# Kernel optimization log

Hardware: AMD Instinct MI355X
Metric: run time of the kernel (lower is better)

Reference implementation:

```python
import jax, jax.numpy as jnp
import numpy as np

C, H, W = 16, 512, 512
HID = 128
N_STEPS = 8


def setup_inputs() -> dict:
    key = jax.random.key(0)
    k1, k2, k3 = jax.random.split(key, 3)
    state = jax.random.normal(k1, (C, H, W), dtype=jnp.float32)
    # MLP params: 5*C = 80 gathered features -> HID -> C delta channels
    W1 = jax.random.normal(k2, (5 * C, HID), dtype=jnp.float32) * (1.0 / np.sqrt(5 * C))
    b1 = jnp.zeros((HID,), dtype=jnp.float32)
    W2 = jax.random.normal(k3, (HID, C), dtype=jnp.float32) * (1.0 / np.sqrt(HID))
    b2 = jnp.zeros((C,), dtype=jnp.float32)
    return {"state": state, "W1": W1, "b1": b1, "W2": W2, "b2": b2, "n_steps": N_STEPS}


def _neighbor_idx(n):
    i = jnp.arange(n)
    minus = jnp.maximum(i - 1, 0)          # clamp at low edge (cy==0 -> 0)
    plus = jnp.where(i == n - 1, 0, i + 1)  # WRAP to 0 at high edge (original quirk)
    return minus, plus


def reference(state, W1, b1, W2, b2, n_steps):
    c, h, w = state.shape
    up, down = _neighbor_idx(h)
    left, right = _neighbor_idx(w)

    def step(s, _):
        # von-Neumann gather: (5C, H, W), feature order [center, up, down, left, right]
        feats = jnp.concatenate(
            [s, s[:, up, :], s[:, down, :], s[:, :, left], s[:, :, right]], axis=0)
        x = feats.reshape(5 * c, h * w).T        # (HW, 5C)
        hdn = jax.nn.relu(x @ W1 + b1)           # (HW, HID)
        delta = (hdn @ W2 + b2).T.reshape(c, h, w)
        s_new = s + delta
        s_new = s_new.at[0].set(s[0])            # channel 0 snapshot restore
        return s_new, None

    out, _ = jax.lax.scan(step, state, None, length=n_steps)
    return out
```

## Files before the change

### kernel.cpp

```cpp
#include <hip/hip_runtime.h>
#include <hip/hip_bf16.h>

#define HH 512
#define WW 512
#define CC 16
#define HIDN 128
#define HWSZ (HH*WW)

typedef __attribute__((ext_vector_type(8))) short short8;
typedef __attribute__((ext_vector_type(4))) short short4v;
typedef __attribute__((ext_vector_type(4))) float float4v;

__device__ __forceinline__ short to_bf16(float f){
    __hip_bfloat16 h = __float2bfloat16(f);
    return __builtin_bit_cast(short, h);
}

__global__ void __launch_bounds__(256) prep_kernel(
    const float* __restrict__ W1, const float* __restrict__ W2,
    short* __restrict__ w1t, short* __restrict__ w2t)
{
    int t = blockIdx.x * blockDim.x + threadIdx.x;
    int stride = gridDim.x * blockDim.x;
    for (int idx = t; idx < HIDN*96; idx += stride){
        int n = idx / 96;
        int k = idx - n*96;
        float v = (k < 80) ? W1[k*HIDN + n] : 0.0f;
        w1t[idx] = to_bf16(v);
    }
    for (int idx = t; idx < CC*HIDN; idx += stride){
        int n = idx >> 7;
        int k = idx & 127;
        w2t[idx] = to_bf16(W2[k*CC + n]);
    }
}

#define RSTRIDE 24
#define RROW    (68*RSTRIDE)

__global__ void __launch_bounds__(256, 5) step_kernel(
    const float* __restrict__ src, float* __restrict__ dst,
    const short* __restrict__ w1t, const short* __restrict__ w2t,
    const float* __restrict__ b1, const float* __restrict__ b2)
{
    __shared__ __align__(16) short rows_u[3*RROW];
    __shared__ __align__(16) short hdn[64][136];
    __shared__ __align__(16) float sctr[64][16];
    __shared__ float b1s[HIDN];
    __shared__ float b2s[CC];

    float (*stg)[65] = (float (*)[65])rows_u;

    const int t    = threadIdx.x;
    const int w    = t >> 6;
    const int lane = t & 63;
    const int ln15 = lane & 15;
    const int g4   = lane >> 4;

    const int bx = blockIdx.x;
    const int y  = bx >> 3;
    const int xs = (bx & 7) << 6;

    if (t < HIDN) b1s[t] = b1[t];
    if (t < CC)   b2s[t] = b2[t];

    const int yu = (y == 0)      ? 0 : (y - 1);
    const int yd = (y == HH - 1) ? 0 : (y + 1);

    if (t < 192){
        const int r  = t >> 6;
        const int l  = t & 63;
        const int q  = l & 15;
        const int cq = l >> 4;
        const int rowg = (r == 0) ? y : ((r == 1) ? yu : yd);
        const float* base = src + (size_t)rowg * WW + xs + (q << 2);
        float4v f[4];
        #pragma unroll
        for (int i = 0; i < 4; ++i)
            f[i] = *(const float4v*)(base + (size_t)((cq << 2) + i) * HWSZ);
        #pragma unroll
        for (int j = 0; j < 4; ++j){
            short4v v;
            v[0] = to_bf16(f[0][j]); v[1] = to_bf16(f[1][j]);
            v[2] = to_bf16(f[2][j]); v[3] = to_bf16(f[3][j]);
            *(short4v*)&rows_u[r*RROW + ((q << 2) + 1 + j)*RSTRIDE + (cq << 2)] = v;
            if (r == 0){
                float4v g = {f[0][j], f[1][j], f[2][j], f[3][j]};
                *(float4v*)&sctr[(q << 2) + j][cq << 2] = g;
            }
        }
    } else if (t < 224){
        const int c    = (t - 192) & 15;
        const int side = (t - 192) >> 4;
        const int gx   = (side == 0) ? ((xs == 0) ? 0 : xs - 1)
                                     : ((xs + 64 == WW) ? 0 : xs + 64);
        rows_u[(side * 65)*RSTRIDE + c] =
            to_bf16(src[(size_t)c*HWSZ + (size_t)y*WW + gx]);
    }
    __syncthreads();

    int offA[3];
    #pragma unroll
    for (int kk = 0; kk < 3; ++kk){
        const int g  = (kk < 2) ? ((kk << 2) + g4) : (8 + (g4 & 1));
        const int n  = g >> 1;
        const int cb = (g & 1) << 3;
        const int r  = (n == 1) ? 1 : ((n == 2) ? 2 : 0);
        const int dx = (n == 3) ? -1 : ((n == 4) ? 1 : 0);
        offA[kk] = r*RROW + (ln15 + 1 + dx)*RSTRIDE + cb;
    }

    float4v acc[4][2];
    #pragma unroll
    for (int mt = 0; mt < 4; ++mt)
        #pragma unroll
        for (int nt = 0; nt < 2; ++nt)
            acc[mt][nt] = (float4v){0.f, 0.f, 0.f, 0.f};

    #pragma unroll
    for (int kk = 0; kk < 3; ++kk){
        short8 bfrag[2];
        #pragma unroll
        for (int nt = 0; nt < 2; ++nt){
            const int col = (w << 5) + (nt << 4) + ln15;
            bfrag[nt] = *(const short8*)(w1t + col * 96 + (kk << 5) + (g4 << 3));
        }
        #pragma unroll
        for (int mt = 0; mt < 4; ++mt){
            short8 afrag = *(const short8*)(&rows_u[offA[kk] + mt * (16 * RSTRIDE)]);
            #pragma unroll
            for (int nt = 0; nt < 2; ++nt){
                acc[mt][nt] = __builtin_amdgcn_mfma_f32_16x16x32_bf16(
                    afrag, bfrag[nt], acc[mt][nt], 0, 0, 0);
            }
        }
    }

    #pragma unroll
    for (int nt = 0; nt < 2; ++nt){
        const int col  = (w << 5) + (nt << 4) + ln15;
        const float bias = b1s[col];
        #pragma unroll
        for (int mt = 0; mt < 4; ++mt){
            #pragma unroll
            for (int r = 0; r < 4; ++r){
                const int m = (mt << 4) + (g4 << 2) + r;
                float v = acc[mt][nt][r] + bias;
                v = v > 0.f ? v : 0.f;
                hdn[m][col] = to_bf16(v);
            }
        }
    }
    __syncthreads();

    float4v acc2 = (float4v){0.f, 0.f, 0.f, 0.f};
    #pragma unroll
    for (int kk = 0; kk < 4; ++kk){
        const int k0 = kk << 5;
        short8 a = *(const short8*)(&hdn[(w << 4) + ln15][k0 + (g4 << 3)]);
        short8 b = *(const short8*)(w2t + ln15 * HIDN + k0 + (g4 << 3));
        acc2 = __builtin_amdgcn_mfma_f32_16x16x32_bf16(a, b, acc2, 0, 0, 0);
    }

    {
        const int c = ln15;
        const float bias2 = b2s[c];
        #pragma unroll
        for (int r = 0; r < 4; ++r){
            const int p = (w << 4) + (g4 << 2) + r;
            const float sold = sctr[p][c];
            float v = (c == 0) ? sold : (sold + acc2[r] + bias2);
            stg[c][p] = v;
        }
    }
    __syncthreads();

    #pragma unroll
    for (int i = 0; i < 4; ++i){
        const int idx = t + (i << 8);
        const int c2  = idx >> 6;
        const int xo  = idx & 63;
        dst[(size_t)c2 * HWSZ + (size_t)y * WW + xs + xo] = stg[c2][xo];
    }
}

extern "C" void kernel_launch(void* const* d_in, const int* in_sizes, int n_in,
                              void* d_out, int out_size, void* d_ws, size_t ws_size,
                              hipStream_t stream)
{
    const float* state = (const float*)d_in[0];
    const float* W1    = (const float*)d_in[1];
    const float* b1    = (const float*)d_in[2];
    const float* W2    = (const float*)d_in[3];
    const float* b2    = (const float*)d_in[4];

    float* B1  = (float*)d_ws;
    short* w1t = (short*)((char*)d_ws + (size_t)HWSZ * CC * 4);
    short* w2t = w1t + HIDN * 96;
    float* out = (float*)d_out;

    prep_kernel<<<32, 256, 0, stream>>>(W1, W2, w1t, w2t);

    dim3 grid(HH * (WW / 64));
    step_kernel<<<grid, 256, 0, stream>>>(state, B1, w1t, w2t, b1, b2);
    step_kernel<<<grid, 256, 0, stream>>>(B1, out, w1t, w2t, b1, b2);
    step_kernel<<<grid, 256, 0, stream>>>(out, B1, w1t, w2t, b1, b2);
    step_kernel<<<grid, 256, 0, stream>>>(B1, out, w1t, w2t, b1, b2);
    step_kernel<<<grid, 256, 0, stream>>>(out, B1, w1t, w2t, b1, b2);
    step_kernel<<<grid, 256, 0, stream>>>(B1, out, w1t, w2t, b1, b2);
    step_kernel<<<grid, 256, 0, stream>>>(out, B1, w1t, w2t, b1, b2);
    step_kernel<<<grid, 256, 0, stream>>>(B1, out, w1t, w2t, b1, b2);
}
```

Measured before the change: 262.6 us.

## Fuse all steps into one persistent cooperative kernel with grid syncs

Measured after the change: 677.7 us. +158.0%, slower.

```diff
diff --git a/kernel.cpp b/kernel.cpp
--- a/kernel.cpp
+++ b/kernel.cpp
@@ -1,5 +1,8 @@
 #include <hip/hip_runtime.h>
 #include <hip/hip_bf16.h>
+#include <hip/hip_cooperative_groups.h>
+
+namespace cg = cooperative_groups;
 
 #define HH 512
 #define WW 512
@@ -15,6 +18,10 @@
     __hip_bfloat16 h = __float2bfloat16(f);
     return __builtin_bit_cast(short, h);
 }
+
+#define RSTRIDE 24
+#define RROW    (68*RSTRIDE)
+
 
 __global__ void __launch_bounds__(256) prep_kernel(
     const float* __restrict__ W1, const float* __restrict__ W2,
@@ -35,38 +42,16 @@
     }
 }
 
-#define RSTRIDE 24
-#define RROW    (68*RSTRIDE)
-
-__global__ void __launch_bounds__(256, 5) step_kernel(
+template<bool HAVE_WFRAGS>
+__device__ __forceinline__ void do_strip(
     const float* __restrict__ src, float* __restrict__ dst,
     const short* __restrict__ w1t, const short* __restrict__ w2t,
-    const float* __restrict__ b1, const float* __restrict__ b2)
-{
-    __shared__ __align__(16) short rows_u[3*RROW];
-    __shared__ __align__(16) short hdn[64][136];
-    __shared__ __align__(16) float sctr[64][16];
-    __shared__ float b1s[HIDN];
-    __shared__ float b2s[CC];
-
-    float (*stg)[65] = (float (*)[65])rows_u;
-
-    const int t    = threadIdx.x;
-    const int w    = t >> 6;
-    const int lane = t & 63;
-    const int ln15 = lane & 15;
-    const int g4   = lane >> 4;
-
-    const int bx = blockIdx.x;
-    const int y  = bx >> 3;
-    const int xs = (bx & 7) << 6;
-
-    if (t < HIDN) b1s[t] = b1[t];
-    if (t < CC)   b2s[t] = b2[t];
-
-    const int yu = (y == 0)      ? 0 : (y - 1);
-    const int yd = (y == HH - 1) ? 0 : (y + 1);
-
+    short (*rows_u), short (*hdn)[136], float (*sctr)[16],
+    float (*stg)[65], const float* b1s, const float* b2s,
+    int t, int w, int lane, int ln15, int g4,
+    int y, int xs, int yu, int yd,
+    const int* offA, const short8 (*bf1)[2], const short8* bf2)
+{
     if (t < 192){
         const int r  = t >> 6;
         const int l  = t & 63;
@@ -99,17 +84,6 @@
     }
     __syncthreads();
 
-    int offA[3];
-    #pragma unroll
-    for (int kk = 0; kk < 3; ++kk){
-        const int g  = (kk < 2) ? ((kk << 2) + g4) : (8 + (g4 & 1));
-        const int n  = g >> 1;
-        const int cb = (g & 1) << 3;
-        const int r  = (n == 1) ? 1 : ((n == 2) ? 2 : 0);
-        const int dx = (n == 3) ? -1 : ((n == 4) ? 1 : 0);
-        offA[kk] = r*RROW + (ln15 + 1 + dx)*RSTRIDE + cb;
-    }
-
     float4v acc[4][2];
     #pragma unroll
     for (int mt = 0; mt < 4; ++mt)
@@ -120,10 +94,14 @@
     #pragma unroll
     for (int kk = 0; kk < 3; ++kk){
         short8 bfrag[2];
-        #pragma unroll
-        for (int nt = 0; nt < 2; ++nt){
-            const int col = (w << 5) + (nt << 4) + ln15;
-            bfrag[nt] = *(const short8*)(w1t + col * 96 + (kk << 5) + (g4 << 3));
+        if (HAVE_WFRAGS){
+            bfrag[0] = bf1[kk][0]; bfrag[1] = bf1[kk][1];
+        } else {
+            #pragma unroll
+            for (int nt = 0; nt < 2; ++nt){
+                const int col = (w << 5) + (nt << 4) + ln15;
+                bfrag[nt] = *(const short8*)(w1t + col * 96 + (kk << 5) + (g4 << 3));
+            }
         }
         #pragma unroll
         for (int mt = 0; mt < 4; ++mt){
@@ -156,9 +134,10 @@
     float4v acc2 = (float4v){0.f, 0.f, 0.f, 0.f};
     #pragma unroll
     for (int kk = 0; kk < 4; ++kk){
-        const int k0 = kk << 5;
-        short8 a = *(const short8*)(&hdn[(w << 4) + ln15][k0 + (g4 << 3)]);
-        short8 b = *(const short8*)(w2t + ln15 * HIDN + k0 + (g4 << 3));
+        short8 a = *(const short8*)(&hdn[(w << 4) + ln15][(kk << 5) + (g4 << 3)]);
+        short8 b;
+        if (HAVE_WFRAGS) b = bf2[kk];
+        else b = *(const short8*)(w2t + ln15 * HIDN + (kk << 5) + (g4 << 3));
         acc2 = __builtin_amdgcn_mfma_f32_16x16x32_bf16(a, b, acc2, 0, 0, 0);
     }
 
@@ -184,6 +163,128 @@
     }
 }
 
+__device__ __forceinline__ void make_offA(int* offA, int ln15, int g4){
+    #pragma unroll
+    for (int kk = 0; kk < 3; ++kk){
+        const int g  = (kk < 2) ? ((kk << 2) + g4) : (8 + (g4 & 1));
+        const int n  = g >> 1;
+        const int cb = (g & 1) << 3;
+        const int r  = (n == 1) ? 1 : ((n == 2) ? 2 : 0);
+        const int dx = (n == 3) ? -1 : ((n == 4) ? 1 : 0);
+        offA[kk] = r*RROW + (ln15 + 1 + dx)*RSTRIDE + cb;
+    }
+}
+
+__global__ void __launch_bounds__(256, 5) step_kernel(
+    const float* __restrict__ src, float* __restrict__ dst,
+    const short* __restrict__ w1t, const short* __restrict__ w2t,
+    const float* __restrict__ b1, const float* __restrict__ b2)
+{
+    __shared__ __align__(16) short rows_u[3*RROW];
+    __shared__ __align__(16) short hdn[64][136];
+    __shared__ __align__(16) float sctr[64][16];
+    __shared__ float b1s[HIDN];
+    __shared__ float b2s[CC];
+    float (*stg)[65] = (float (*)[65])rows_u;
+
+    const int t    = threadIdx.x;
+    const int w    = t >> 6;
+    const int lane = t & 63;
+    const int ln15 = lane & 15;
+    const int g4   = lane >> 4;
+    const int bx   = blockIdx.x;
+    const int y    = bx >> 3;
+    const int xs   = (bx & 7) << 6;
+
+    if (t < HIDN) b1s[t] = b1[t];
+    if (t < CC)   b2s[t] = b2[t];
+
+    const int yu = (y == 0)      ? 0 : (y - 1);
+    const int yd = (y == HH - 1) ? 0 : (y + 1);
+
+    int offA[3];
+    make_offA(offA, ln15, g4);
+
+    do_strip<false>(src, dst, w1t, w2t, rows_u, hdn, sctr, stg, b1s, b2s,
+                    t, w, lane, ln15, g4, y, xs, yu, yd, offA, nullptr, nullptr);
+}
+
+__global__ void __launch_bounds__(256, 2) fused_kernel(
+    const float* __restrict__ state, float* __restrict__ out,
+    float* __restrict__ B1,
+    short* __restrict__ w1t, short* __restrict__ w2t,
+    const float* __restrict__ W1, const float* __restrict__ W2,
+    const float* __restrict__ b1, const float* __restrict__ b2)
+{
+    __shared__ __align__(16) short rows_u[3*RROW];
+    __shared__ __align__(16) short hdn[64][136];
+    __shared__ __align__(16) float sctr[64][16];
+    __shared__ float b1s[HIDN];
+    __shared__ float b2s[CC];
+    float (*stg)[65] = (float (*)[65])rows_u;
+
+    const int t    = threadIdx.x;
+    const int w    = t >> 6;
+    const int lane = t & 63;
+    const int ln15 = lane & 15;
+    const int g4   = lane >> 4;
+    const int bid  = blockIdx.x;
+
+    cg::grid_group grid = cg::this_grid();
+
+    if (bid < 32){
+        const int gt = (bid << 8) + t;
+        for (int idx = gt; idx < HIDN*96; idx += 8192){
+            int n = idx / 96;
+            int k = idx - n*96;
+            float v = (k < 80) ? W1[k*HIDN + n] : 0.0f;
+            w1t[idx] = to_bf16(v);
+        }
+        for (int idx = gt; idx < CC*HIDN; idx += 8192){
+            int n = idx >> 7;
+            int k = idx & 127;
+            w2t[idx] = to_bf16(W2[k*CC + n]);
+        }
+    }
+    if (t < HIDN) b1s[t] = b1[t];
+    if (t < CC)   b2s[t] = b2[t];
+    grid.sync();
+
+    short8 bf1[3][2];
+    #pragma unroll
+    for (int kk = 0; kk < 3; ++kk)
+        #pragma unroll
+        for (int nt = 0; nt < 2; ++nt){
+            const int col = (w << 5) + (nt << 4) + ln15;
+            bf1[kk][nt] = *(const short8*)(w1t + col * 96 + (kk << 5) + (g4 << 3));
+        }
+    short8 bf2[4];
+    #pragma unroll
+    for (int kk = 0; kk < 4; ++kk)
+        bf2[kk] = *(const short8*)(w2t + ln15 * HIDN + (kk << 5) + (g4 << 3));
+
+    int offA[3];
+    make_offA(offA, ln15, g4);
+
+    const int y  = ((bid & 7) << 6) + (bid >> 3);
+    const int yu = (y == 0)      ? 0 : (y - 1);
+    const int yd = (y == HH - 1) ? 0 : (y + 1);
+
+    for (int s = 0; s < 8; ++s){
+        if (s) grid.sync();
+        const float* __restrict__ src = (s == 0) ? state : ((s & 1) ? B1 : out);
+        float* __restrict__ dst       = (s & 1) ? out : B1;
+
+        #pragma unroll 1
+        for (int cs = 0; cs < 8; ++cs){
+            const int xs = cs << 6;
+            do_strip<true>(src, dst, w1t, w2t, rows_u, hdn, sctr, stg, b1s, b2s,
+                           t, w, lane, ln15, g4, y, xs, yu, yd, offA, bf1, bf2);
+            __syncthreads();
+        }
+    }
+}
+
 extern "C" void kernel_launch(void* const* d_in, const int* in_sizes, int n_in,
                               void* d_out, int out_size, void* d_ws, size_t ws_size,
                               hipStream_t stream)
@@ -199,15 +300,21 @@
     short* w2t = w1t + HIDN * 96;
     float* out = (float*)d_out;
 
-    prep_kernel<<<32, 256, 0, stream>>>(W1, W2, w1t, w2t);
-
-    dim3 grid(HH * (WW / 64));
-    step_kernel<<<grid, 256, 0, stream>>>(state, B1, w1t, w2t, b1, b2);
-    step_kernel<<<grid, 256, 0, stream>>>(B1, out, w1t, w2t, b1, b2);
-    step_kernel<<<grid, 256, 0, stream>>>(out, B1, w1t, w2t, b1, b2);
-    step_kernel<<<grid, 256, 0, stream>>>(B1, out, w1t, w2t, b1, b2);
-    step_kernel<<<grid, 256, 0, stream>>>(out, B1, w1t, w2t, b1, b2);
-    step_kernel<<<grid, 256, 0, stream>>>(B1, out, w1t, w2t, b1, b2);
-    step_kernel<<<grid, 256, 0, stream>>>(out, B1, w1t, w2t, b1, b2);
-    step_kernel<<<grid, 256, 0, stream>>>(B1, out, w1t, w2t, b1, b2);
-}
+    void* args[] = { (void*)&state, (void*)&out, (void*)&B1,
+                     (void*)&w1t, (void*)&w2t, (void*)&W1, (void*)&W2,
+                     (void*)&b1, (void*)&b2 };
+    hipError_t e = hipLaunchCooperativeKernel((const void*)fused_kernel,
+                                              dim3(512), dim3(256), args, 0, stream);
+    if (e != hipSuccess){
+        prep_kernel<<<32, 256, 0, stream>>>(W1, W2, w1t, w2t);
+        dim3 grid(HH * (WW / 64));
+        step_kernel<<<grid, 256, 0, stream>>>(state, B1, w1t, w2t, b1, b2);
+        step_kernel<<<grid, 256, 0, stream>>>(B1, out, w1t, w2t, b1, b2);
+        step_kernel<<<grid, 256, 0, stream>>>(out, B1, w1t, w2t, b1, b2);
+        step_kernel<<<grid, 256, 0, stream>>>(B1, out, w1t, w2t, b1, b2);
+        step_kernel<<<grid, 256, 0, stream>>>(out, B1, w1t, w2t, b1, b2);
+        step_kernel<<<grid, 256, 0, stream>>>(B1, out, w1t, w2t, b1, b2);
+        step_kernel<<<grid, 256, 0, stream>>>(out, B1, w1t, w2t, b1, b2);
+        step_kernel<<<grid, 256, 0, stream>>>(B1, out, w1t, w2t, b1, b2);
+    }
+}
```

## Remap blocks per XCD, swizzle LDS rows, retile GEMM1 warps, load residual directly

Applied to the files above, without the earlier changes.

New measurement: 284.7 us. +8.4%, slower.

```diff
diff --git a/kernel.cpp b/kernel.cpp
--- a/kernel.cpp
+++ b/kernel.cpp
@@ -15,6 +15,9 @@
     __hip_bfloat16 h = __float2bfloat16(f);
     return __builtin_bit_cast(short, h);
 }
+
+#define RSTRIDE 24
+#define RROW    (68*RSTRIDE)
 
 __global__ void __launch_bounds__(256) prep_kernel(
     const float* __restrict__ W1, const float* __restrict__ W2,
@@ -35,9 +38,6 @@
     }
 }
 
-#define RSTRIDE 24
-#define RROW    (68*RSTRIDE)
-
 __global__ void __launch_bounds__(256, 5) step_kernel(
     const float* __restrict__ src, float* __restrict__ dst,
     const short* __restrict__ w1t, const short* __restrict__ w2t,
@@ -45,10 +45,8 @@
 {
     __shared__ __align__(16) short rows_u[3*RROW];
     __shared__ __align__(16) short hdn[64][136];
-    __shared__ __align__(16) float sctr[64][16];
     __shared__ float b1s[HIDN];
     __shared__ float b2s[CC];
-
     float (*stg)[65] = (float (*)[65])rows_u;
 
     const int t    = threadIdx.x;
@@ -57,15 +55,26 @@
     const int ln15 = lane & 15;
     const int g4   = lane >> 4;
 
-    const int bx = blockIdx.x;
-    const int y  = bx >> 3;
-    const int xs = (bx & 7) << 6;
+    const int bid = blockIdx.x;
+    const int xcd = bid & 7;
+    const int i   = bid >> 3;
+    const int y   = (xcd << 6) + (i >> 3);
+    const int xs  = (i & 7) << 6;
+
+    const int yu = (y == 0)      ? 0 : (y - 1);
+    const int yd = (y == HH - 1) ? 0 : (y + 1);
+
+    float res[4];
+    #pragma unroll
+    for (int ii = 0; ii < 4; ++ii){
+        const int idx = t + (ii << 8);
+        const int c2  = idx >> 6;
+        const int xo  = idx & 63;
+        res[ii] = src[(size_t)c2 * HWSZ + (size_t)y * WW + xs + xo];
+    }
 
     if (t < HIDN) b1s[t] = b1[t];
     if (t < CC)   b2s[t] = b2[t];
-
-    const int yu = (y == 0)      ? 0 : (y - 1);
-    const int yd = (y == HH - 1) ? 0 : (y + 1);
 
     if (t < 192){
         const int r  = t >> 6;
@@ -76,18 +85,17 @@
         const float* base = src + (size_t)rowg * WW + xs + (q << 2);
         float4v f[4];
         #pragma unroll
-        for (int i = 0; i < 4; ++i)
-            f[i] = *(const float4v*)(base + (size_t)((cq << 2) + i) * HWSZ);
+        for (int ii = 0; ii < 4; ++ii)
+            f[ii] = *(const float4v*)(base + (size_t)((cq << 2) + ii) * HWSZ);
         #pragma unroll
         for (int j = 0; j < 4; ++j){
+            const int xl   = (q << 2) + 1 + j;
+            const int key  = (xl >> 3) & 1;
+            const int slot = (cq >> 1) ^ key;
             short4v v;
             v[0] = to_bf16(f[0][j]); v[1] = to_bf16(f[1][j]);
             v[2] = to_bf16(f[2][j]); v[3] = to_bf16(f[3][j]);
-            *(short4v*)&rows_u[r*RROW + ((q << 2) + 1 + j)*RSTRIDE + (cq << 2)] = v;
-            if (r == 0){
-                float4v g = {f[0][j], f[1][j], f[2][j], f[3][j]};
-                *(float4v*)&sctr[(q << 2) + j][cq << 2] = g;
-            }
+            *(short4v*)&rows_u[r*RROW + xl*RSTRIDE + (slot << 3) + ((cq & 1) << 2)] = v;
         }
     } else if (t < 224){
         const int c    = (t - 192) & 15;
@@ -104,32 +112,35 @@
     for (int kk = 0; kk < 3; ++kk){
         const int g  = (kk < 2) ? ((kk << 2) + g4) : (8 + (g4 & 1));
         const int n  = g >> 1;
-        const int cb = (g & 1) << 3;
+        const int oc = g & 1;
         const int r  = (n == 1) ? 1 : ((n == 2) ? 2 : 0);
         const int dx = (n == 3) ? -1 : ((n == 4) ? 1 : 0);
-        offA[kk] = r*RROW + (ln15 + 1 + dx)*RSTRIDE + cb;
-    }
-
-    float4v acc[4][2];
-    #pragma unroll
-    for (int mt = 0; mt < 4; ++mt)
-        #pragma unroll
-        for (int nt = 0; nt < 2; ++nt)
+        const int xl = ln15 + 1 + dx;
+        const int key = (xl >> 3) & 1;
+        offA[kk] = r*RROW + xl*RSTRIDE + ((oc ^ key) << 3);
+    }
+
+    const int wm = w & 1, wn = w >> 1;
+    float4v acc[2][4];
+    #pragma unroll
+    for (int mt = 0; mt < 2; ++mt)
+        #pragma unroll
+        for (int nt = 0; nt < 4; ++nt)
             acc[mt][nt] = (float4v){0.f, 0.f, 0.f, 0.f};
 
     #pragma unroll
     for (int kk = 0; kk < 3; ++kk){
-        short8 bfrag[2];
-        #pragma unroll
-        for (int nt = 0; nt < 2; ++nt){
-            const int col = (w << 5) + (nt << 4) + ln15;
+        short8 bfrag[4];
+        #pragma unroll
+        for (int nt = 0; nt < 4; ++nt){
+            const int col = (wn << 6) + (nt << 4) + ln15;
             bfrag[nt] = *(const short8*)(w1t + col * 96 + (kk << 5) + (g4 << 3));
         }
         #pragma unroll
-        for (int mt = 0; mt < 4; ++mt){
-            short8 afrag = *(const short8*)(&rows_u[offA[kk] + mt * (16 * RSTRIDE)]);
+        for (int mt = 0; mt < 2; ++mt){
+            short8 afrag = *(const short8*)(&rows_u[offA[kk] + ((wm << 5) + (mt << 4)) * RSTRIDE]);
             #pragma unroll
-            for (int nt = 0; nt < 2; ++nt){
+            for (int nt = 0; nt < 4; ++nt){
                 acc[mt][nt] = __builtin_amdgcn_mfma_f32_16x16x32_bf16(
                     afrag, bfrag[nt], acc[mt][nt], 0, 0, 0);
             }
@@ -137,14 +148,14 @@
     }
 
     #pragma unroll
-    for (int nt = 0; nt < 2; ++nt){
-        const int col  = (w << 5) + (nt << 4) + ln15;
+    for (int nt = 0; nt < 4; ++nt){
+        const int col  = (wn << 6) + (nt << 4) + ln15;
         const float bias = b1s[col];
         #pragma unroll
-        for (int mt = 0; mt < 4; ++mt){
+        for (int mt = 0; mt < 2; ++mt){
             #pragma unroll
             for (int r = 0; r < 4; ++r){
-                const int m = (mt << 4) + (g4 << 2) + r;
+                const int m = (wm << 5) + (mt << 4) + (g4 << 2) + r;
                 float v = acc[mt][nt][r] + bias;
                 v = v > 0.f ? v : 0.f;
                 hdn[m][col] = to_bf16(v);
@@ -156,31 +167,29 @@
     float4v acc2 = (float4v){0.f, 0.f, 0.f, 0.f};
     #pragma unroll
     for (int kk = 0; kk < 4; ++kk){
-        const int k0 = kk << 5;
-        short8 a = *(const short8*)(&hdn[(w << 4) + ln15][k0 + (g4 << 3)]);
-        short8 b = *(const short8*)(w2t + ln15 * HIDN + k0 + (g4 << 3));
+        short8 a = *(const short8*)(&hdn[(w << 4) + ln15][(kk << 5) + (g4 << 3)]);
+        short8 b = *(const short8*)(w2t + ln15 * HIDN + (kk << 5) + (g4 << 3));
         acc2 = __builtin_amdgcn_mfma_f32_16x16x32_bf16(a, b, acc2, 0, 0, 0);
     }
 
     {
         const int c = ln15;
         const float bias2 = b2s[c];
-        #pragma unroll
-        for (int r = 0; r < 4; ++r){
-            const int p = (w << 4) + (g4 << 2) + r;
-            const float sold = sctr[p][c];
-            float v = (c == 0) ? sold : (sold + acc2[r] + bias2);
-            stg[c][p] = v;
-        }
+        const int p0 = (w << 4) + (g4 << 2);
+        #pragma unroll
+        for (int r = 0; r < 4; ++r)
+            stg[c][p0 + r] = acc2[r] + bias2;
     }
     __syncthreads();
 
     #pragma unroll
-    for (int i = 0; i < 4; ++i){
-        const int idx = t + (i << 8);
+    for (int ii = 0; ii < 4; ++ii){
+        const int idx = t + (ii << 8);
         const int c2  = idx >> 6;
         const int xo  = idx & 63;
-        dst[(size_t)c2 * HWSZ + (size_t)y * WW + xs + xo] = stg[c2][xo];
+        float v = res[ii];
+        if (c2 != 0) v += stg[c2][xo];
+        dst[(size_t)c2 * HWSZ + (size_t)y * WW + xs + xo] = v;
     }
 }
 
```
